# Kernel optimization log

Measured on AMD Instinct MI355X. Metric: run time of the kernel, lower is better.

Reference implementation:

```python
import jax, jax.numpy as jnp
import numpy as np

B, K, T, C, F = 2048, 32, 365, 4, 128  # batch, prototypes, steps, bands, feature_size


def conv1d(x, w, b, pad):
    # x: (B, Cin, T), w: (Cout, Cin, Kw)
    y = jax.lax.conv_general_dilated(x, w, (1,), [(pad, pad)],
                                     dimension_numbers=('NCH', 'OIH', 'NCH'))
    return y + b[None, :, None]


def bn_relu(x, gamma, beta):
    # training-mode BatchNorm1d over (batch, time) per channel
    mu = x.mean((0, 2), keepdims=True)
    var = x.var((0, 2), keepdims=True)
    xn = (x - mu) * jax.lax.rsqrt(var + 1e-5)
    return jax.nn.relu(xn * gamma[None, :, None] + beta[None, :, None])


def encoder(x, w1, b1, g1, be1, w2, b2, g2, be2, w3, b3, g3, be3, fc_w, fc_b):
    # FCNBaseline: 3 conv blocks + global average pool + linear
    h = x.transpose(0, 2, 1)                    # (B, C, T)
    h = bn_relu(conv1d(h, w1, b1, 4), g1, be1)  # (B, 128, T+1)
    h = bn_relu(conv1d(h, w2, b2, 2), g2, be2)  # (B, 256, *)
    h = bn_relu(conv1d(h, w3, b3, 1), g3, be3)  # (B, 128, *)
    return h.mean(-1) @ fc_w.T + fc_b           # (B, F)


def setup_inputs() -> dict:
    key = jax.random.key(0)
    ks = jax.random.split(key, 12)
    input_seq = jax.random.normal(ks[0], (B, T, C), jnp.float32)
    label = jax.random.randint(ks[1], (B,), 0, 9)
    mask = (jax.random.uniform(ks[2], (B, T)) > 0.2).astype(jnp.float32)
    prototypes = jax.random.normal(ks[3], (K, T, C), jnp.float32)
    w1 = jax.random.normal(ks[4], (128, C, 8)) * 0.05
    b1 = jnp.zeros((128,)); g1 = jnp.ones((128,)); be1 = jnp.zeros((128,))
    w2 = jax.random.normal(ks[5], (256, 128, 5)) * 0.05
    b2 = jnp.zeros((256,)); g2 = jnp.ones((256,)); be2 = jnp.zeros((256,))
    w3 = jax.random.normal(ks[6], (128, 256, 3)) * 0.05
    b3 = jnp.zeros((128,)); g3 = jnp.ones((128,)); be3 = jnp.zeros((128,))
    fc_w = jax.random.normal(ks[7], (F, 128)) * 0.05
    fc_b = jnp.zeros((F,))
    off_w = jax.random.normal(ks[8], (K * C, F)) * 0.05
    off_b = jnp.zeros((K * C,))
    return dict(input_seq=input_seq, label=label, mask=mask, prototypes=prototypes,
                w1=w1, b1=b1, g1=g1, be1=be1, w2=w2, b2=b2, g2=g2, be2=be2,
                w3=w3, b3=b3, g3=g3, be3=be3, fc_w=fc_w, fc_b=fc_b,
                off_w=off_w, off_b=off_b)


def reference(input_seq, label, mask, prototypes, w1, b1, g1, be1, w2, b2, g2, be2,
              w3, b3, g3, be3, fc_w, fc_b, off_w, off_b):
    # trans_activ=False (TPS warp disabled), offset_activ=True, unsupervised path
    feat = encoder(input_seq, w1, b1, g1, be1, w2, b2, g2, be2, w3, b3, g3, be3, fc_w, fc_b)
    offset = jnp.tanh(feat @ off_w.T + off_b).reshape(-1, K, 1, C)  # (B,K,1,C)
    protos = prototypes[None] + offset                              # (B,K,T,C)
    diff = input_seq[:, None] - protos                              # (B,K,T,C)
    # masked squared-distance reduce: mask (B,T) broadcasts over (K,C)
    distances = jnp.einsum('bktc,bt->bk', diff * diff, mask)        # (B,K)
    indices = jnp.argmin(distances, axis=1)                         # (B,)
    output_seq = jnp.take_along_axis(protos, indices[:, None, None, None], axis=1)[:, 0]
    return output_seq
```

## Files before the change

kernel.cpp:

```cpp
#include <hip/hip_runtime.h>
#include <hip/hip_bf16.h>

#define BB 2048
#define TIN 365
#define TO 366
#define C1 128
#define C2 256
#define C3 128
#define FF 128

typedef __attribute__((ext_vector_type(4))) float f32x4v;
typedef __attribute__((ext_vector_type(8))) short bf16x8;

__device__ inline unsigned short f2bf(float v) {
  unsigned u = __float_as_uint(v);
  unsigned r = (u + 0x7FFF + ((u >> 16) & 1)) >> 16;
  return (unsigned short)r;
}
__device__ inline float bf2f(unsigned short b) {
  return __uint_as_float(((unsigned)b) << 16);
}

__global__ void wprep2_kernel(const float* __restrict__ w2,
                              short* __restrict__ wh, short* __restrict__ wl) {
  int n = 256 * 128 * 5;
  for (int idx = blockIdx.x * 256 + threadIdx.x; idx < n; idx += gridDim.x * 256) {
    int k = idx % 5;
    int rest = idx / 5;
    int i = rest % 128;
    int o = rest / 128;
    float v = w2[idx];
    unsigned short hb = f2bf(v);
    unsigned short lb = f2bf(v - bf2f(hb));
    size_t dst = ((((size_t)k * 4 + (i >> 5)) * 16 + (o >> 4)) * 64 +
                  ((i >> 3) & 3) * 16 + (o & 15)) * 8 + (i & 7);
    wh[dst] = (short)hb;
    wl[dst] = (short)lb;
  }
}
__global__ void wprep3_kernel(const float* __restrict__ w3,
                              short* __restrict__ wh, short* __restrict__ wl) {
  int n = 128 * 256 * 3;
  for (int idx = blockIdx.x * 256 + threadIdx.x; idx < n; idx += gridDim.x * 256) {
    int k = idx % 3;
    int rest = idx / 3;
    int i = rest % 256;
    int o = rest / 256;
    float v = w3[idx];
    unsigned short hb = f2bf(v);
    unsigned short lb = f2bf(v - bf2f(hb));
    size_t dst = ((((size_t)k * 8 + (i >> 5)) * 8 + (o >> 4)) * 64 +
                  ((i >> 3) & 3) * 16 + (o & 15)) * 8 + (i & 7);
    wh[dst] = (short)hb;
    wl[dst] = (short)lb;
  }
}

__global__ void bnparam_kernel(const double* __restrict__ sums,
                               const float* __restrict__ gamma,
                               const float* __restrict__ beta, int Cch,
                               float* __restrict__ scale, float* __restrict__ shift) {
  int i = threadIdx.x;
  if (i < Cch) {
    const double N = (double)BB * (double)TO;
    double mean = sums[i] / N;
    double var = sums[Cch + i] / N - mean * mean;
    double sc = (double)gamma[i] / sqrt(var + 1e-5);
    scale[i] = (float)sc;
    shift[i] = (float)((double)beta[i] - mean * sc);
  }
}

__global__ __launch_bounds__(256) void conv1_stats_kernel(
    const float* __restrict__ x, const float* __restrict__ w1,
    const float* __restrict__ b1, double* __restrict__ sums) {
  __shared__ float4 xs[374];
  __shared__ float ws1[4096];
  int tid = threadIdx.x;
  for (int i = tid; i < 4096; i += 256) ws1[i] = w1[i];
  __syncthreads();
  const int o = tid >> 1, half = tid & 1;
  float wr[32];
#pragma unroll
  for (int i = 0; i < 32; ++i) wr[i] = ws1[o * 32 + i];
  const float bo = b1[o];
  float s1 = 0.f, s2 = 0.f;
  for (int b = blockIdx.x * 8; b < blockIdx.x * 8 + 8; ++b) {
    __syncthreads();
    for (int u = tid; u < 374; u += 256) {
      int t_in = u - 4;
      float4 v = make_float4(0.f, 0.f, 0.f, 0.f);
      if (t_in >= 0 && t_in < TIN) v = *(const float4*)(x + ((size_t)b * TIN + t_in) * 4);
      xs[u] = v;
    }
    __syncthreads();
    for (int t = half * 183; t < half * 183 + 183; ++t) {
      float acc = bo;
#pragma unroll
      for (int k = 0; k < 8; ++k) {
        float4 xv = xs[t + k];
        acc = fmaf(wr[k], xv.x, acc);
        acc = fmaf(wr[8 + k], xv.y, acc);
        acc = fmaf(wr[16 + k], xv.z, acc);
        acc = fmaf(wr[24 + k], xv.w, acc);
      }
      s1 += acc; s2 += acc * acc;
    }
  }
  s1 += __shfl_xor(s1, 1);
  s2 += __shfl_xor(s2, 1);
  if (half == 0) {
    atomicAdd(&sums[o], (double)s1);
    atomicAdd(&sums[C1 + o], (double)s2);
  }
}

__global__ __launch_bounds__(256) void conv2_mfma_kernel(
    const float* __restrict__ x, const float* __restrict__ w1g,
    const float* __restrict__ b1, const float* __restrict__ scale1,
    const float* __restrict__ shift1, const short* __restrict__ w2ph,
    const short* __restrict__ w2pl, const float* __restrict__ b2,
    float* __restrict__ p2) {
  __shared__ float ws1[4096];
  __shared__ float4 xwin[76];
  __shared__ __align__(16) short h1h[68 * 72];
  __shared__ __align__(16) short h1l[68 * 72];
  __shared__ float sstat[512];
  const int tid = threadIdx.x;
  const int tt = blockIdx.x, b = blockIdx.y;
  const int tbase = tt * 64;
  const int slice = (b * 6 + tt) & 63;
  const int w = tid >> 6, lane = tid & 63;
  const int q = lane >> 4, l15 = lane & 15;

  for (int i = tid; i < 4096; i += 256) ws1[i] = w1g[i];
  for (int u = tid; u < 76; u += 256) {
    int tx = tbase - 6 + u;
    float4 v = make_float4(0.f, 0.f, 0.f, 0.f);
    if (tx >= 0 && tx < TIN) v = *(const float4*)(x + ((size_t)b * TIN + tx) * 4);
    xwin[u] = v;
  }
  float b2r[4][4];
#pragma unroll
  for (int om = 0; om < 4; ++om)
#pragma unroll
    for (int r = 0; r < 4; ++r) b2r[om][r] = b2[64 * w + om * 16 + q * 4 + r];

  f32x4v acc[4][4];
#pragma unroll
  for (int om = 0; om < 4; ++om)
#pragma unroll
    for (int nt = 0; nt < 4; ++nt) acc[om][nt] = (f32x4v){0.f, 0.f, 0.f, 0.f};

  const int chl = tid >> 2, qt = tid & 3;
  for (int ic2 = 0; ic2 < 2; ++ic2) {
    __syncthreads();
    {
      int ch = ic2 * 64 + chl;
      float sc = scale1[ch], sh = shift1[ch], bo = b1[ch];
      const float* wr = &ws1[ch * 32];
      for (int j = 0; j < 17; ++j) {
        int u = qt * 17 + j;
        int t = tbase - 2 + u;
        float a = bo;
#pragma unroll
        for (int kk = 0; kk < 8; ++kk) {
          float4 xv = xwin[u + kk];
          a = fmaf(wr[kk], xv.x, a);
          a = fmaf(wr[8 + kk], xv.y, a);
          a = fmaf(wr[16 + kk], xv.z, a);
          a = fmaf(wr[24 + kk], xv.w, a);
        }
        float v = (t >= 0 && t < TO) ? fmaxf(fmaf(sc, a, sh), 0.f) : 0.f;
        unsigned short hb = f2bf(v);
        h1h[u * 72 + chl] = (short)hb;
        h1l[u * 72 + chl] = (short)f2bf(v - bf2f(hb));
      }
    }
    __syncthreads();
    for (int k = 0; k < 5; ++k) {
      for (int ic = 0; ic < 2; ++ic) {
        int icg = ic2 * 2 + ic;
        bf16x8 ah[4], al[4];
#pragma unroll
        for (int om = 0; om < 4; ++om) {
          int og = 4 * w + om;
          size_t base = ((((size_t)k * 4 + icg) * 16 + og) * 64 + lane) * 8;
          ah[om] = *(const bf16x8*)(w2ph + base);
          al[om] = *(const bf16x8*)(w2pl + base);
        }
        int ioff = ic * 32 + q * 8;
#pragma unroll
        for (int nt = 0; nt < 4; ++nt) {
          int u = nt * 16 + l15 + k;
          bf16x8 bh = *(const bf16x8*)&h1h[u * 72 + ioff];
          bf16x8 bl = *(const bf16x8*)&h1l[u * 72 + ioff];
#pragma unroll
          for (int om = 0; om < 4; ++om) {
            acc[om][nt] = __builtin_amdgcn_mfma_f32_16x16x32_bf16(ah[om], bh, acc[om][nt], 0, 0, 0);
            acc[om][nt] = __builtin_amdgcn_mfma_f32_16x16x32_bf16(ah[om], bl, acc[om][nt], 0, 0, 0);
            acc[om][nt] = __builtin_amdgcn_mfma_f32_16x16x32_bf16(al[om], bh, acc[om][nt], 0, 0, 0);
          }
        }
      }
    }
  }
  float ts1[16], ts2[16];
#pragma unroll
  for (int i = 0; i < 16; ++i) { ts1[i] = 0.f; ts2[i] = 0.f; }
#pragma unroll
  for (int om = 0; om < 4; ++om)
#pragma unroll
    for (int nt = 0; nt < 4; ++nt) {
      int t = tbase + nt * 16 + l15;
      if (t < TO) {
#pragma unroll
        for (int r = 0; r < 4; ++r) {
          float v = acc[om][nt][r] + b2r[om][r];
          ts1[om * 4 + r] += v;
          ts2[om * 4 + r] += v * v;
        }
      }
    }
#pragma unroll
  for (int i = 0; i < 16; ++i) {
#pragma unroll
    for (int d = 1; d < 16; d <<= 1) {
      ts1[i] += __shfl_xor(ts1[i], d);
      ts2[i] += __shfl_xor(ts2[i], d);
    }
  }
  if (l15 == 0) {
#pragma unroll
    for (int om = 0; om < 4; ++om)
#pragma unroll
      for (int r = 0; r < 4; ++r) {
        int o = 64 * w + om * 16 + q * 4 + r;
        sstat[o] = ts1[om * 4 + r];
        sstat[256 + o] = ts2[om * 4 + r];
      }
  }
  __syncthreads();
  atomicAdd(&p2[(size_t)tid * 64 + slice], sstat[tid]);
  atomicAdd(&p2[((size_t)tid + 256) * 64 + slice], sstat[tid + 256]);
}

template <int EPI, bool STOREH3>
__global__ __launch_bounds__(256) void fused23_kernel(
    const float* __restrict__ x, const float* __restrict__ w1g,
    const float* __restrict__ b1, const float* __restrict__ scale1,
    const float* __restrict__ shift1, const short* __restrict__ w2ph,
    const short* __restrict__ w2pl, const float* __restrict__ b2,
    const float* __restrict__ scale2, const float* __restrict__ shift2,
    const short* __restrict__ w3ph, const short* __restrict__ w3pl,
    const float* __restrict__ b3, const float* __restrict__ scale3,
    const float* __restrict__ shift3, float* __restrict__ p3,
    float* __restrict__ pooled, float* __restrict__ h3g) {
  __shared__ float4 xwin[80];
  __shared__ __align__(16) short un[34848];
  __shared__ float bn2s[768];
  __shared__ float sstat[256];
  short* h1h = un;
  short* h1l = un + 70 * 72;
  short* h2sh = un;
  short* h2sl = un + 66 * 264;
  const int tid = threadIdx.x;
  const int tt = blockIdx.x, b = blockIdx.y;
  const int tbase = tt * 64;
  const int slice = (b * 6 + tt) & 63;
  const int w = tid >> 6, lane = tid & 63;
  const int q = lane >> 4, l15 = lane & 15;

  for (int u = tid; u < 77; u += 256) {
    int tx = tbase - 7 + u;
    float4 v = make_float4(0.f, 0.f, 0.f, 0.f);
    if (tx >= 0 && tx < TIN) v = *(const float4*)(x + ((size_t)b * TIN + tx) * 4);
    xwin[u] = v;
  }
  bn2s[tid] = b2[tid];
  bn2s[256 + tid] = scale2[tid];
  bn2s[512 + tid] = shift2[tid];

  float b3r[2][4], sc3r[2][4], sh3r[2][4];
#pragma unroll
  for (int om = 0; om < 2; ++om)
#pragma unroll
    for (int r = 0; r < 4; ++r) {
      int o = 32 * w + om * 16 + q * 4 + r;
      b3r[om][r] = b3[o];
      if (EPI == 1) { sc3r[om][r] = scale3[o]; sh3r[om][r] = shift3[o]; }
    }

  f32x4v acc2[4][5];
#pragma unroll
  for (int om = 0; om < 4; ++om)
#pragma unroll
    for (int nt = 0; nt < 5; ++nt) acc2[om][nt] = (f32x4v){0.f, 0.f, 0.f, 0.f};

  const int chl = tid >> 2, qt = tid & 3;
  for (int ic2 = 0; ic2 < 2; ++ic2) {
    int ch = ic2 * 64 + chl;
    float wr[32];
#pragma unroll
    for (int i = 0; i < 32; ++i) wr[i] = w1g[ch * 32 + i];
    float sc = scale1[ch], sh = shift1[ch], bo = b1[ch];
    __syncthreads();
    for (int j = 0; j < 18; ++j) {
      int u1 = qt * 18 + j;
      if (u1 < 70) {
        int t1 = tbase - 3 + u1;
        float a = bo;
#pragma unroll
        for (int kk = 0; kk < 8; ++kk) {
          float4 xv = xwin[u1 + kk];
          a = fmaf(wr[kk], xv.x, a);
          a = fmaf(wr[8 + kk], xv.y, a);
          a = fmaf(wr[16 + kk], xv.z, a);
          a = fmaf(wr[24 + kk], xv.w, a);
        }
        float v = (t1 >= 0 && t1 < TO) ? fmaxf(fmaf(sc, a, sh), 0.f) : 0.f;
        unsigned short hb = f2bf(v);
        h1h[u1 * 72 + chl] = (short)hb;
        h1l[u1 * 72 + chl] = (short)f2bf(v - bf2f(hb));
      }
    }
    __syncthreads();
    for (int k = 0; k < 5; ++k) {
      for (int ic = 0; ic < 2; ++ic) {
        int icg = ic2 * 2 + ic;
        bf16x8 ah[4], al[4];
#pragma unroll
        for (int om = 0; om < 4; ++om) {
          int og = 4 * w + om;
          size_t base = ((((size_t)k * 4 + icg) * 16 + og) * 64 + lane) * 8;
          ah[om] = *(const bf16x8*)(w2ph + base);
          al[om] = *(const bf16x8*)(w2pl + base);
        }
        int ioff = ic * 32 + q * 8;
#pragma unroll
        for (int nt = 0; nt < 5; ++nt) {
          int u1 = nt * 16 + l15 + k;
          if (u1 > 69) u1 = 69;
          bf16x8 bh = *(const bf16x8*)&h1h[u1 * 72 + ioff];
          bf16x8 bl = *(const bf16x8*)&h1l[u1 * 72 + ioff];
#pragma unroll
          for (int om = 0; om < 4; ++om) {
            acc2[om][nt] = __builtin_amdgcn_mfma_f32_16x16x32_bf16(ah[om], bh, acc2[om][nt], 0, 0, 0);
            acc2[om][nt] = __builtin_amdgcn_mfma_f32_16x16x32_bf16(ah[om], bl, acc2[om][nt], 0, 0, 0);
            acc2[om][nt] = __builtin_amdgcn_mfma_f32_16x16x32_bf16(al[om], bh, acc2[om][nt], 0, 0, 0);
          }
        }
      }
    }
  }
  __syncthreads();
#pragma unroll
  for (int om = 0; om < 4; ++om) {
    int og = 4 * w + om;
#pragma unroll
    for (int nt = 0; nt < 5; ++nt) {
      int u2 = nt * 16 + l15;
      if (u2 < 66) {
        int t2 = tbase - 1 + u2;
        bool valid = (t2 >= 0 && t2 < TO);
#pragma unroll
        for (int rp = 0; rp < 2; ++rp) {
          int o = og * 16 + q * 4 + rp * 2;
          float v0 = 0.f, v1 = 0.f;
          if (valid) {
            v0 = fmaxf(fmaf(bn2s[256 + o], acc2[om][nt][rp * 2] + bn2s[o], bn2s[512 + o]), 0.f);
            v1 = fmaxf(fmaf(bn2s[256 + o + 1], acc2[om][nt][rp * 2 + 1] + bn2s[o + 1], bn2s[512 + o + 1]), 0.f);
          }
          unsigned short hb0 = f2bf(v0), hb1 = f2bf(v1);
          *(unsigned*)&h2sh[u2 * 264 + o] = (unsigned)hb0 | ((unsigned)hb1 << 16);
          *(unsigned*)&h2sl[u2 * 264 + o] =
              (unsigned)f2bf(v0 - bf2f(hb0)) | ((unsigned)f2bf(v1 - bf2f(hb1)) << 16);
        }
      }
    }
  }
  __syncthreads();
  f32x4v acc3[2][4];
#pragma unroll
  for (int om = 0; om < 2; ++om)
#pragma unroll
    for (int nt = 0; nt < 4; ++nt) acc3[om][nt] = (f32x4v){0.f, 0.f, 0.f, 0.f};
  for (int k = 0; k < 3; ++k) {
    for (int icg = 0; icg < 8; ++icg) {
      bf16x8 a3h[2], a3l[2];
#pragma unroll
      for (int om = 0; om < 2; ++om) {
        int og = 2 * w + om;
        size_t base = ((((size_t)k * 8 + icg) * 8 + og) * 64 + lane) * 8;
        a3h[om] = *(const bf16x8*)(w3ph + base);
        a3l[om] = *(const bf16x8*)(w3pl + base);
      }
      int ioff = icg * 32 + q * 8;
#pragma unroll
      for (int nt = 0; nt < 4; ++nt) {
        int u = nt * 16 + l15 + k;
        bf16x8 bh = *(const bf16x8*)&h2sh[u * 264 + ioff];
        bf16x8 bl = *(const bf16x8*)&h2sl[u * 264 + ioff];
#pragma unroll
        for (int om = 0; om < 2; ++om) {
          acc3[om][nt] = __builtin_amdgcn_mfma_f32_16x16x32_bf16(a3h[om], bh, acc3[om][nt], 0, 0, 0);
          acc3[om][nt] = __builtin_amdgcn_mfma_f32_16x16x32_bf16(a3l[om], bh, acc3[om][nt], 0, 0, 0);
          acc3[om][nt] = __builtin_amdgcn_mfma_f32_16x16x32_bf16(a3h[om], bl, acc3[om][nt], 0, 0, 0);
        }
      }
    }
  }
  if (EPI == 0) {
    float ts1[8], ts2[8];
#pragma unroll
    for (int i = 0; i < 8; ++i) { ts1[i] = 0.f; ts2[i] = 0.f; }
#pragma unroll
    for (int om = 0; om < 2; ++om)
#pragma unroll
      for (int nt = 0; nt < 4; ++nt) {
        int t = tbase + nt * 16 + l15;
        if (t < TO) {
#pragma unroll
          for (int r = 0; r < 4; ++r) {
            float v = acc3[om][nt][r] + b3r[om][r];
            ts1[om * 4 + r] += v;
            ts2[om * 4 + r] += v * v;
            if (STOREH3) {
              int o = 32 * w + om * 16 + q * 4 + r;
              h3g[((size_t)b * 128 + o) * 368 + t] = v;
            }
          }
        }
      }
#pragma unroll
    for (int i = 0; i < 8; ++i) {
#pragma unroll
      for (int d = 1; d < 16; d <<= 1) {
        ts1[i] += __shfl_xor(ts1[i], d);
        ts2[i] += __shfl_xor(ts2[i], d);
      }
    }
    if (l15 == 0) {
#pragma unroll
      for (int om = 0; om < 2; ++om)
#pragma unroll
        for (int r = 0; r < 4; ++r) {
          int o = 32 * w + om * 16 + q * 4 + r;
          sstat[o] = ts1[om * 4 + r];
          sstat[128 + o] = ts2[om * 4 + r];
        }
    }
    __syncthreads();
    atomicAdd(&p3[(size_t)tid * 64 + slice], sstat[tid]);
  } else {
    float ps[8];
#pragma unroll
    for (int i = 0; i < 8; ++i) ps[i] = 0.f;
#pragma unroll
    for (int om = 0; om < 2; ++om)
#pragma unroll
      for (int nt = 0; nt < 4; ++nt) {
        int t = tbase + nt * 16 + l15;
        if (t < TO) {
#pragma unroll
          for (int r = 0; r < 4; ++r) {
            float v = acc3[om][nt][r] + b3r[om][r];
            ps[om * 4 + r] += fmaxf(fmaf(sc3r[om][r], v, sh3r[om][r]), 0.f);
          }
        }
      }
#pragma unroll
    for (int i = 0; i < 8; ++i) {
#pragma unroll
      for (int d = 1; d < 16; d <<= 1) ps[i] += __shfl_xor(ps[i], d);
    }
    if (l15 == 0) {
#pragma unroll
      for (int om = 0; om < 2; ++om)
#pragma unroll
        for (int r = 0; r < 4; ++r) {
          int o = 32 * w + om * 16 + q * 4 + r;
          atomicAdd(&pooled[(size_t)b * 128 + o], ps[om * 4 + r]);
        }
    }
  }
}

__global__ __launch_bounds__(256) void gap3_kernel(
    const float* __restrict__ h3g, const float* __restrict__ scale3,
    const float* __restrict__ shift3, float* __restrict__ pooled) {
  int b = blockIdx.x, tid = threadIdx.x;
  int w = tid >> 6, lane = tid & 63;
  for (int cc = 0; cc < 32; ++cc) {
    int ch = w * 32 + cc;
    float sc = scale3[ch], sh = shift3[ch];
    const float* row = h3g + ((size_t)b * 128 + ch) * 368;
    float s = 0.f;
    for (int u = lane; u < TO; u += 64)
      s += fmaxf(fmaf(sc, row[u], sh), 0.f);
#pragma unroll
    for (int d = 32; d > 0; d >>= 1) s += __shfl_xor(s, d);
    if (lane == 0) pooled[(size_t)b * 128 + ch] = s;
  }
}

__global__ __launch_bounds__(64) void reduce_slices_kernel(
    const float* __restrict__ p, double* __restrict__ sums) {
  int c = blockIdx.x, tid = threadIdx.x;
  double s = (double)p[(size_t)c * 64 + tid];
  for (int d = 32; d > 0; d >>= 1) s += __shfl_down(s, d);
  if (tid == 0) sums[c] = s;
}

__global__ __launch_bounds__(128) void head2_kernel(
    const float* __restrict__ pooled, const float* __restrict__ fc_w,
    const float* __restrict__ fc_b, const float* __restrict__ off_w,
    const float* __restrict__ off_b, float* __restrict__ offs) {
  int b = blockIdx.x, tid = threadIdx.x;
  __shared__ float pl[128], feat[128];
  pl[tid] = pooled[(size_t)b * C3 + tid] * (1.0f / 366.0f);
  __syncthreads();
  {
    const float* wr = fc_w + tid * FF;
    float a = fc_b[tid];
    for (int i = 0; i < 128; ++i) a = fmaf(pl[i], wr[i], a);
    feat[tid] = a;
  }
  __syncthreads();
  {
    const float* wr = off_w + tid * FF;
    float z = off_b[tid];
    for (int i = 0; i < 128; ++i) z = fmaf(feat[i], wr[i], z);
    offs[(size_t)b * 128 + tid] = tanhf(z);
  }
}

__global__ __launch_bounds__(256) void dist_kernel(
    const float* __restrict__ x, const float* __restrict__ mask,
    const float* __restrict__ protos, const float* __restrict__ offs,
    float* __restrict__ out) {
  int b = blockIdx.x, tid = threadIdx.x;
  __shared__ float ofl[128];
  __shared__ double dred[256];
  __shared__ int ksel;
  if (tid < 128) ofl[tid] = offs[(size_t)b * 128 + tid];
  __syncthreads();
  int k = tid & 31, tg = tid >> 5;
  float o0 = ofl[k * 4 + 0], o1 = ofl[k * 4 + 1], o2 = ofl[k * 4 + 2], o3 = ofl[k * 4 + 3];
  double acc = 0.0;
  for (int t = tg; t < TIN; t += 8) {
    float4 xv = *(const float4*)(x + ((size_t)b * TIN + t) * 4);
    float4 pv = *(const float4*)(protos + ((size_t)k * TIN + t) * 4);
    float m = mask[(size_t)b * TIN + t];
    float d0 = xv.x - pv.x - o0;
    float d1 = xv.y - pv.y - o1;
    float d2 = xv.z - pv.z - o2;
    float d3 = xv.w - pv.w - o3;
    acc += (double)(m * (d0 * d0 + d1 * d1 + d2 * d2 + d3 * d3));
  }
  dred[tid] = acc;
  __syncthreads();
  if (tid < 32) {
    double s = 0.0;
    for (int g = 0; g < 8; ++g) s += dred[g * 32 + tid];
    dred[tid] = s;
  }
  __syncthreads();
  if (tid == 0) {
    double best = dred[0]; int bi = 0;
    for (int kk = 1; kk < 32; ++kk)
      if (dred[kk] < best) { best = dred[kk]; bi = kk; }
    ksel = bi;
  }
  __syncthreads();
  int km = ksel;
  const float* psrc = protos + (size_t)km * TIN * 4;
  float* dst = out + (size_t)b * TIN * 4;
  for (int u = tid; u < TIN * 4; u += 256)
    dst[u] = psrc[u] + ofl[km * 4 + (u & 3)];
}

extern "C" void kernel_launch(void* const* d_in, const int* in_sizes, int n_in,
                              void* d_out, int out_size, void* d_ws, size_t ws_size,
                              hipStream_t stream) {
  const float* x      = (const float*)d_in[0];
  const float* mask   = (const float*)d_in[2];
  const float* protos = (const float*)d_in[3];
  const float* w1 = (const float*)d_in[4];
  const float* b1 = (const float*)d_in[5];
  const float* g1 = (const float*)d_in[6];
  const float* be1 = (const float*)d_in[7];
  const float* w2 = (const float*)d_in[8];
  const float* b2 = (const float*)d_in[9];
  const float* g2 = (const float*)d_in[10];
  const float* be2 = (const float*)d_in[11];
  const float* w3 = (const float*)d_in[12];
  const float* b3 = (const float*)d_in[13];
  const float* g3 = (const float*)d_in[14];
  const float* be3 = (const float*)d_in[15];
  const float* fc_w = (const float*)d_in[16];
  const float* fc_b = (const float*)d_in[17];
  const float* off_w = (const float*)d_in[18];
  const float* off_b = (const float*)d_in[19];
  float* out = (float*)d_out;
  (void)in_sizes; (void)n_in; (void)out_size;

  char* wsp = (char*)d_ws;
  size_t off = 0;
  auto alloc = [&](size_t bytes) { void* p = wsp + off; off += (bytes + 255) & ~(size_t)255; return p; };
  float* bnp   = (float*)alloc(1024 * 4);
  float* offs  = (float*)alloc((size_t)BB * 128 * 4);
  size_t zero_beg = off;
  double* sums  = (double*)alloc(1024 * 8);
  float* pooled = (float*)alloc((size_t)BB * C3 * 4);
  float* p2     = (float*)alloc((size_t)512 * 64 * 4);
  float* p3     = (float*)alloc((size_t)256 * 64 * 4);
  size_t zero_end = off;
  short* w2ph = (short*)alloc((size_t)256 * 128 * 5 * 2);
  short* w2pl = (short*)alloc((size_t)256 * 128 * 5 * 2);
  short* w3ph = (short*)alloc((size_t)128 * 256 * 3 * 2);
  short* w3pl = (short*)alloc((size_t)128 * 256 * 3 * 2);
  size_t small_end = off;
  const size_t h3_bytes = (size_t)BB * 128 * 368 * 4;
  float* h3g = (float*)(wsp + small_end);
  const bool h3_ok = ws_size >= small_end + h3_bytes;

  double* sums1 = sums;
  double* sums2 = sums + 256;
  double* sums3 = sums + 768;
  float* scale1 = bnp;        float* shift1 = bnp + 128;
  float* scale2 = bnp + 256;  float* shift2 = bnp + 512;
  float* scale3 = bnp + 768;  float* shift3 = bnp + 896;

  hipMemsetAsync(wsp + zero_beg, 0, zero_end - zero_beg, stream);

  conv1_stats_kernel<<<256, 256, 0, stream>>>(x, w1, b1, sums1);
  bnparam_kernel<<<1, 256, 0, stream>>>(sums1, g1, be1, C1, scale1, shift1);

  wprep2_kernel<<<256, 256, 0, stream>>>(w2, w2ph, w2pl);
  wprep3_kernel<<<128, 256, 0, stream>>>(w3, w3ph, w3pl);

  conv2_mfma_kernel<<<dim3(6, BB), 256, 0, stream>>>(
      x, w1, b1, scale1, shift1, w2ph, w2pl, b2, p2);
  reduce_slices_kernel<<<512, 64, 0, stream>>>(p2, sums2);
  bnparam_kernel<<<1, 256, 0, stream>>>(sums2, g2, be2, C2, scale2, shift2);

  if (h3_ok) {
    fused23_kernel<0, true><<<dim3(6, BB), 256, 0, stream>>>(
        x, w1, b1, scale1, shift1, w2ph, w2pl, b2, scale2, shift2,
        w3ph, w3pl, b3, scale3, shift3, p3, pooled, h3g);
    reduce_slices_kernel<<<256, 64, 0, stream>>>(p3, sums3);
    bnparam_kernel<<<1, 256, 0, stream>>>(sums3, g3, be3, C3, scale3, shift3);
    gap3_kernel<<<BB, 256, 0, stream>>>(h3g, scale3, shift3, pooled);
  } else {
    fused23_kernel<0, false><<<dim3(6, BB), 256, 0, stream>>>(
        x, w1, b1, scale1, shift1, w2ph, w2pl, b2, scale2, shift2,
        w3ph, w3pl, b3, scale3, shift3, p3, pooled, h3g);
    reduce_slices_kernel<<<256, 64, 0, stream>>>(p3, sums3);
    bnparam_kernel<<<1, 256, 0, stream>>>(sums3, g3, be3, C3, scale3, shift3);
    fused23_kernel<1, false><<<dim3(6, BB), 256, 0, stream>>>(
        x, w1, b1, scale1, shift1, w2ph, w2pl, b2, scale2, shift2,
        w3ph, w3pl, b3, scale3, shift3, p3, pooled, h3g);
  }

  head2_kernel<<<BB, 128, 0, stream>>>(pooled, fc_w, fc_b, off_w, off_b, offs);
  dist_kernel<<<BB, 256, 0, stream>>>(x, mask, protos, offs, out);
}
```

Measured before the change: 3.873 ms.

## Halve fused conv2/conv3 LDS via two-pass channel split; partially cache h3

The conv3 stage now stages the h2 activation in LDS in two halves of 128 channels. Each half is written, then consumed by the conv3 MFMA loop, which halves the shared-memory footprint of the fused kernel so more blocks can be resident per CU. The cost is an extra barrier and the h1/acc2 live range across both passes, which may raise register pressure. Separately, h3 is now cached for as many batches as the workspace can hold. Only the remaining batches are recomputed in the second-pass kernel, replacing the previous all-or-nothing choice.

```diff
diff --git a/kernel.cpp b/kernel.cpp
--- a/kernel.cpp
+++ b/kernel.cpp
@@ -245,7 +245,7 @@
   atomicAdd(&p2[((size_t)tid + 256) * 64 + slice], sstat[tid + 256]);
 }
 
-template <int EPI, bool STOREH3>
+template <int EPI>
 __global__ __launch_bounds__(256) void fused23_kernel(
     const float* __restrict__ x, const float* __restrict__ w1g,
     const float* __restrict__ b1, const float* __restrict__ scale1,
@@ -255,17 +255,19 @@
     const short* __restrict__ w3ph, const short* __restrict__ w3pl,
     const float* __restrict__ b3, const float* __restrict__ scale3,
     const float* __restrict__ shift3, float* __restrict__ p3,
-    float* __restrict__ pooled, float* __restrict__ h3g) {
+    float* __restrict__ pooled, float* __restrict__ h3g,
+    int bstore, int boff) {
   __shared__ float4 xwin[80];
-  __shared__ __align__(16) short un[34848];
+  __shared__ __align__(16) short un[17424];
   __shared__ float bn2s[768];
   __shared__ float sstat[256];
   short* h1h = un;
   short* h1l = un + 70 * 72;
   short* h2sh = un;
-  short* h2sl = un + 66 * 264;
+  short* h2sl = un + 66 * 132;
   const int tid = threadIdx.x;
-  const int tt = blockIdx.x, b = blockIdx.y;
+  const int tt = blockIdx.x;
+  const int b = blockIdx.y + boff;
   const int tbase = tt * 64;
   const int slice = (b * 6 + tt) & 63;
   const int w = tid >> 6, lane = tid & 63;
@@ -354,58 +356,64 @@
     }
   }
   __syncthreads();
-#pragma unroll
-  for (int om = 0; om < 4; ++om) {
-    int og = 4 * w + om;
-#pragma unroll
-    for (int nt = 0; nt < 5; ++nt) {
-      int u2 = nt * 16 + l15;
-      if (u2 < 66) {
-        int t2 = tbase - 1 + u2;
-        bool valid = (t2 >= 0 && t2 < TO);
-#pragma unroll
-        for (int rp = 0; rp < 2; ++rp) {
-          int o = og * 16 + q * 4 + rp * 2;
-          float v0 = 0.f, v1 = 0.f;
-          if (valid) {
-            v0 = fmaxf(fmaf(bn2s[256 + o], acc2[om][nt][rp * 2] + bn2s[o], bn2s[512 + o]), 0.f);
-            v1 = fmaxf(fmaf(bn2s[256 + o + 1], acc2[om][nt][rp * 2 + 1] + bn2s[o + 1], bn2s[512 + o + 1]), 0.f);
+  f32x4v acc3[2][4];
+#pragma unroll
+  for (int om = 0; om < 2; ++om)
+#pragma unroll
+    for (int nt = 0; nt < 4; ++nt) acc3[om][nt] = (f32x4v){0.f, 0.f, 0.f, 0.f};
+  for (int c = 0; c < 2; ++c) {
+    if (c) __syncthreads();
+#pragma unroll
+    for (int ml = 0; ml < 2; ++ml) {
+      int om = 2 * c + ml;
+      int og = 4 * w + om;
+#pragma unroll
+      for (int nt = 0; nt < 5; ++nt) {
+        int u2 = nt * 16 + l15;
+        if (u2 < 66) {
+          int t2 = tbase - 1 + u2;
+          bool valid = (t2 >= 0 && t2 < TO);
+#pragma unroll
+          for (int rp = 0; rp < 2; ++rp) {
+            int o = og * 16 + q * 4 + rp * 2;
+            int ol = (w * 2 + ml) * 16 + q * 4 + rp * 2;
+            float v0 = 0.f, v1 = 0.f;
+            if (valid) {
+              v0 = fmaxf(fmaf(bn2s[256 + o], acc2[om][nt][rp * 2] + bn2s[o], bn2s[512 + o]), 0.f);
+              v1 = fmaxf(fmaf(bn2s[256 + o + 1], acc2[om][nt][rp * 2 + 1] + bn2s[o + 1], bn2s[512 + o + 1]), 0.f);
+            }
+            unsigned short hb0 = f2bf(v0), hb1 = f2bf(v1);
+            *(unsigned*)&h2sh[u2 * 132 + ol] = (unsigned)hb0 | ((unsigned)hb1 << 16);
+            *(unsigned*)&h2sl[u2 * 132 + ol] =
+                (unsigned)f2bf(v0 - bf2f(hb0)) | ((unsigned)f2bf(v1 - bf2f(hb1)) << 16);
           }
-          unsigned short hb0 = f2bf(v0), hb1 = f2bf(v1);
-          *(unsigned*)&h2sh[u2 * 264 + o] = (unsigned)hb0 | ((unsigned)hb1 << 16);
-          *(unsigned*)&h2sl[u2 * 264 + o] =
-              (unsigned)f2bf(v0 - bf2f(hb0)) | ((unsigned)f2bf(v1 - bf2f(hb1)) << 16);
-        }
-      }
-    }
-  }
-  __syncthreads();
-  f32x4v acc3[2][4];
-#pragma unroll
-  for (int om = 0; om < 2; ++om)
-#pragma unroll
-    for (int nt = 0; nt < 4; ++nt) acc3[om][nt] = (f32x4v){0.f, 0.f, 0.f, 0.f};
-  for (int k = 0; k < 3; ++k) {
-    for (int icg = 0; icg < 8; ++icg) {
-      bf16x8 a3h[2], a3l[2];
-#pragma unroll
-      for (int om = 0; om < 2; ++om) {
-        int og = 2 * w + om;
-        size_t base = ((((size_t)k * 8 + icg) * 8 + og) * 64 + lane) * 8;
-        a3h[om] = *(const bf16x8*)(w3ph + base);
-        a3l[om] = *(const bf16x8*)(w3pl + base);
-      }
-      int ioff = icg * 32 + q * 8;
-#pragma unroll
-      for (int nt = 0; nt < 4; ++nt) {
-        int u = nt * 16 + l15 + k;
-        bf16x8 bh = *(const bf16x8*)&h2sh[u * 264 + ioff];
-        bf16x8 bl = *(const bf16x8*)&h2sl[u * 264 + ioff];
+        }
+      }
+    }
+    __syncthreads();
+    for (int k = 0; k < 3; ++k) {
+      for (int e = 0; e < 4; ++e) {
+        int icg = c + 2 * e;
+        bf16x8 a3h[2], a3l[2];
 #pragma unroll
         for (int om = 0; om < 2; ++om) {
-          acc3[om][nt] = __builtin_amdgcn_mfma_f32_16x16x32_bf16(a3h[om], bh, acc3[om][nt], 0, 0, 0);
-          acc3[om][nt] = __builtin_amdgcn_mfma_f32_16x16x32_bf16(a3l[om], bh, acc3[om][nt], 0, 0, 0);
-          acc3[om][nt] = __builtin_amdgcn_mfma_f32_16x16x32_bf16(a3h[om], bl, acc3[om][nt], 0, 0, 0);
+          int og = 2 * w + om;
+          size_t base = ((((size_t)k * 8 + icg) * 8 + og) * 64 + lane) * 8;
+          a3h[om] = *(const bf16x8*)(w3ph + base);
+          a3l[om] = *(const bf16x8*)(w3pl + base);
+        }
+        int ioff = e * 32 + q * 8;
+#pragma unroll
+        for (int nt = 0; nt < 4; ++nt) {
+          int u = nt * 16 + l15 + k;
+          bf16x8 bh = *(const bf16x8*)&h2sh[u * 132 + ioff];
+          bf16x8 bl = *(const bf16x8*)&h2sl[u * 132 + ioff];
+#pragma unroll
+          for (int om = 0; om < 2; ++om) {
+            acc3[om][nt] = __builtin_amdgcn_mfma_f32_16x16x32_bf16(a3h[om], bh, acc3[om][nt], 0, 0, 0);
+            acc3[om][nt] = __builtin_amdgcn_mfma_f32_16x16x32_bf16(a3l[om], bh, acc3[om][nt], 0, 0, 0);
+            acc3[om][nt] = __builtin_amdgcn_mfma_f32_16x16x32_bf16(a3h[om], bl, acc3[om][nt], 0, 0, 0);
+          }
         }
       }
     }
@@ -414,6 +422,7 @@
     float ts1[8], ts2[8];
 #pragma unroll
     for (int i = 0; i < 8; ++i) { ts1[i] = 0.f; ts2[i] = 0.f; }
+    bool st = (b < bstore);
 #pragma unroll
     for (int om = 0; om < 2; ++om)
 #pragma unroll
@@ -425,7 +434,7 @@
             float v = acc3[om][nt][r] + b3r[om][r];
             ts1[om * 4 + r] += v;
             ts2[om * 4 + r] += v * v;
-            if (STOREH3) {
+            if (st) {
               int o = 32 * w + om * 16 + q * 4 + r;
               h3g[((size_t)b * 128 + o) * 368 + t] = v;
             }
@@ -621,9 +630,12 @@
   short* w3ph = (short*)alloc((size_t)128 * 256 * 3 * 2);
   short* w3pl = (short*)alloc((size_t)128 * 256 * 3 * 2);
   size_t small_end = off;
-  const size_t h3_bytes = (size_t)BB * 128 * 368 * 4;
   float* h3g = (float*)(wsp + small_end);
-  const bool h3_ok = ws_size >= small_end + h3_bytes;
+  int bstore = 0;
+  if (ws_size > small_end) {
+    size_t cap = (ws_size - small_end) / ((size_t)128 * 368 * 4);
+    bstore = (int)(cap > (size_t)BB ? (size_t)BB : cap);
+  }
 
   double* sums1 = sums;
   double* sums2 = sums + 256;
@@ -645,23 +657,18 @@
   reduce_slices_kernel<<<512, 64, 0, stream>>>(p2, sums2);
   bnparam_kernel<<<1, 256, 0, stream>>>(sums2, g2, be2, C2, scale2, shift2);
 
-  if (h3_ok) {
-    fused23_kernel<0, true><<<dim3(6, BB), 256, 0, stream>>>(
+  fused23_kernel<0><<<dim3(6, BB), 256, 0, stream>>>(
+      x, w1, b1, scale1, shift1, w2ph, w2pl, b2, scale2, shift2,
+      w3ph, w3pl, b3, scale3, shift3, p3, pooled, h3g, bstore, 0);
+  reduce_slices_kernel<<<256, 64, 0, stream>>>(p3, sums3);
+  bnparam_kernel<<<1, 256, 0, stream>>>(sums3, g3, be3, C3, scale3, shift3);
+
+  if (bstore > 0)
+    gap3_kernel<<<bstore, 256, 0, stream>>>(h3g, scale3, shift3, pooled);
+  if (bstore < BB)
+    fused23_kernel<1><<<dim3(6, BB - bstore), 256, 0, stream>>>(
         x, w1, b1, scale1, shift1, w2ph, w2pl, b2, scale2, shift2,
-        w3ph, w3pl, b3, scale3, shift3, p3, pooled, h3g);
-    reduce_slices_kernel<<<256, 64, 0, stream>>>(p3, sums3);
-    bnparam_kernel<<<1, 256, 0, stream>>>(sums3, g3, be3, C3, scale3, shift3);
-    gap3_kernel<<<BB, 256, 0, stream>>>(h3g, scale3, shift3, pooled);
-  } else {
-    fused23_kernel<0, false><<<dim3(6, BB), 256, 0, stream>>>(
-        x, w1, b1, scale1, shift1, w2ph, w2pl, b2, scale2, shift2,
-        w3ph, w3pl, b3, scale3, shift3, p3, pooled, h3g);
-    reduce_slices_kernel<<<256, 64, 0, stream>>>(p3, sums3);
-    bnparam_kernel<<<1, 256, 0, stream>>>(sums3, g3, be3, C3, scale3, shift3);
-    fused23_kernel<1, false><<<dim3(6, BB), 256, 0, stream>>>(
-        x, w1, b1, scale1, shift1, w2ph, w2pl, b2, scale2, shift2,
-        w3ph, w3pl, b3, scale3, shift3, p3, pooled, h3g);
-  }
+        w3ph, w3pl, b3, scale3, shift3, p3, pooled, h3g, 0, bstore);
 
   head2_kernel<<<BB, 128, 0, stream>>>(pooled, fc_w, fc_b, off_w, off_b, offs);
   dist_kernel<<<BB, 256, 0, stream>>>(x, mask, protos, offs, out);
```

Result: slower. 4.501 ms (+16.2%).
